# Kernel optimization log

Measured on AMD Instinct MI355X. Metric: run time of the kernel, lower is better.

## Reference

```python
import jax, jax.numpy as jnp
import numpy as np

B, N, E, H = 4, 512, 512, 8
HD = E // H // 2            # 32; per-head value dim is 2*HD = 64
C_IN = 64                   # u_proj Conv2d in_channels
LAMBDA_INIT = 0.8 - 0.6 * float(np.exp(-0.3 * (28.0 / 28.0) * (1 - 1)))  # layer_idx=1, depth=28 -> 0.2
LN_EPS = 1e-5


def setup_inputs() -> dict:
    key = jax.random.key(0)
    ks = jax.random.split(key, 13)
    x = jax.random.normal(ks[0], (B, N, E), dtype=jnp.float32)
    u = jax.random.normal(ks[1], (B, N, N, C_IN), dtype=jnp.float32)
    umask = jax.random.randint(ks[2], (B, N, N, 2 * H), 0, 2).astype(bool)
    s = 0.02
    v_w = jax.random.normal(ks[3], (E, E), dtype=jnp.float32) * s        # nn.Linear weight [out,in]
    out_w = jax.random.normal(ks[4], (E, E), dtype=jnp.float32) * s
    uproj_w = jax.random.normal(ks[5], (2 * H, C_IN), dtype=jnp.float32) * s  # 1x1 conv kernel
    uproj_b = jax.random.normal(ks[6], (2 * H,), dtype=jnp.float32) * s
    lq1 = jax.random.normal(ks[7], (E,), dtype=jnp.float32) * 0.1
    lk1 = jax.random.normal(ks[8], (E,), dtype=jnp.float32) * 0.1
    lq2 = jax.random.normal(ks[9], (E,), dtype=jnp.float32) * 0.1
    lk2 = jax.random.normal(ks[10], (E,), dtype=jnp.float32) * 0.1
    ln_w = jnp.ones((2 * HD,), dtype=jnp.float32)
    ln_b = jnp.zeros((2 * HD,), dtype=jnp.float32)
    return {"x": x, "u": u, "umask": umask, "v_w": v_w, "out_w": out_w,
            "uproj_w": uproj_w, "uproj_b": uproj_b,
            "lq1": lq1, "lk1": lk1, "lq2": lq2, "lk2": lk2,
            "ln_w": ln_w, "ln_b": ln_b}


def reference(x, u, umask, v_w, out_w, uproj_w, uproj_b, lq1, lk1, lq2, lk2, ln_w, ln_b):
    b, n, e = x.shape
    # v projection -> [B, H, N, 2*HD]
    v = jnp.einsum('bne,fe->bnf', x, v_w).reshape(b, n, H, 2 * HD).transpose(0, 2, 1, 3)
    # 1x1 conv on u: [B,N,N,C_IN] -> [B,N,N,2H]
    ue = jnp.einsum('bnmc,hc->bnmh', u, uproj_w) + uproj_b
    ue = jnp.where(umask, -jnp.inf, ue)
    # transpose(3,1): [B,N,N,2H] -> [B,2H,N,N]; softmax over last (key) axis
    aw = jax.nn.softmax(jnp.transpose(ue, (0, 3, 2, 1)), axis=-1)
    lam1 = jnp.exp(jnp.sum(lq1 * lk1))
    lam2 = jnp.exp(jnp.sum(lq2 * lk2))
    lam = lam1 - lam2 + LAMBDA_INIT
    aw = aw.reshape(b, H, 2, n, n)
    diff = aw[:, :, 0] - lam * aw[:, :, 1]          # [B,H,N,N]
    attn = jnp.einsum('bhnm,bhmd->bhnd', diff, v)   # [B,H,N,2HD]
    # sub-LayerNorm over last dim
    mu = jnp.mean(attn, axis=-1, keepdims=True)
    var = jnp.mean(jnp.square(attn - mu), axis=-1, keepdims=True)
    attn = (attn - mu) * jax.lax.rsqrt(var + LN_EPS) * ln_w + ln_b
    attn = attn.transpose(0, 2, 1, 3).reshape(b, n, e)
    return jnp.einsum('bne,fe->bnf', attn, out_w)
```

## Files before the change

kernel.cpp:

```cpp
#include <hip/hip_runtime.h>
#include <math.h>

typedef _Float16 f16x8 __attribute__((ext_vector_type(8)));
typedef _Float16 f16x4 __attribute__((ext_vector_type(4)));
typedef float    f32x4 __attribute__((ext_vector_type(4)));

constexpr int kB  = 4;
constexpr int kN  = 512;
constexpr int kE  = 512;
constexpr int kH  = 8;
constexpr int kH2 = 16;
constexpr int kC  = 64;
constexpr int kDV = 64;
constexpr float kLamInit = 0.2f;

__global__ __launch_bounds__(256) void prep_kernel(
    const float* __restrict__ x, const float* __restrict__ vw,
    const float* __restrict__ ow,
    const float* __restrict__ lq1, const float* __restrict__ lk1,
    const float* __restrict__ lq2, const float* __restrict__ lk2,
    _Float16* __restrict__ x16, _Float16* __restrict__ w16v,
    _Float16* __restrict__ w16o, float* __restrict__ lam_out) {
  const int bid = blockIdx.x;
  if (bid < 1536) {
    const float* src; _Float16* dst; int base;
    if (bid < 1024)      { src = x;  dst = x16;  base = bid; }
    else if (bid < 1280) { src = vw; dst = w16v; base = bid - 1024; }
    else                 { src = ow; dst = w16o; base = bid - 1280; }
    const int i = base * 256 + threadIdx.x;
    const float4 v = ((const float4*)src)[i];
    union { _Float16 h[4]; uint2 u2; } P;
    P.h[0]=(_Float16)v.x; P.h[1]=(_Float16)v.y;
    P.h[2]=(_Float16)v.z; P.h[3]=(_Float16)v.w;
    *(uint2*)(dst + i * 4) = P.u2;
  } else if (threadIdx.x < 64) {
    float s1 = 0.f, s2 = 0.f;
    for (int i = threadIdx.x; i < kE; i += 64) { s1 += lq1[i]*lk1[i]; s2 += lq2[i]*lk2[i]; }
    #pragma unroll
    for (int o = 32; o; o >>= 1) { s1 += __shfl_xor(s1, o); s2 += __shfl_xor(s2, o); }
    if (threadIdx.x == 0) lam_out[0] = expf(s1) - expf(s2) + kLamInit;
  }
}

__global__ __launch_bounds__(256) void hgemm16f(const _Float16* __restrict__ A16,
                                                const _Float16* __restrict__ W16,
                                                float* __restrict__ C,
                                                int M, int F, int K) {
  const int tid = threadIdx.x, lane = tid & 63, wv = tid >> 6;
  const int l15 = lane & 15, l4 = lane >> 4;
  const int m0 = blockIdx.y * 64 + wv * 16;
  const int f0 = blockIdx.x * 64;
  f32x4 acc[4] = {{0,0,0,0},{0,0,0,0},{0,0,0,0},{0,0,0,0}};
  const _Float16* Ap = A16 + (size_t)(m0 + l15) * K + l4 * 8;
  const _Float16* Wp = W16 + (size_t)(f0 + l15) * K + l4 * 8;
  for (int k0 = 0; k0 < K; k0 += 32) {
    const f16x8 af = *(const f16x8*)(Ap + k0);
    #pragma unroll
    for (int t = 0; t < 4; ++t) {
      const f16x8 bf = *(const f16x8*)(Wp + (size_t)t * 16 * K + k0);
      acc[t] = __builtin_amdgcn_mfma_f32_16x16x32_f16(af, bf, acc[t], 0, 0, 0);
    }
  }
  #pragma unroll
  for (int t = 0; t < 4; ++t)
    #pragma unroll
    for (int r = 0; r < 4; ++r)
      C[(size_t)(m0 + l4 * 4 + r) * F + f0 + t * 16 + l15] = acc[t][r];
}

__global__ __launch_bounds__(256) void hgemmT_v(const _Float16* __restrict__ W16,
                                                const _Float16* __restrict__ X16,
                                                _Float16* __restrict__ Vt) {
  const int tid = threadIdx.x, lane = tid & 63, wv = tid >> 6;
  const int l15 = lane & 15, l4 = lane >> 4;
  const int f0 = blockIdx.y * 64 + wv * 16;
  const int n0 = blockIdx.x * 64;
  f32x4 acc[4] = {{0,0,0,0},{0,0,0,0},{0,0,0,0},{0,0,0,0}};
  const _Float16* Ap = W16 + (size_t)(f0 + l15) * kE + l4 * 8;
  const _Float16* Bp = X16 + (size_t)(n0 + l15) * kE + l4 * 8;
  for (int k0 = 0; k0 < kE; k0 += 32) {
    const f16x8 af = *(const f16x8*)(Ap + k0);
    #pragma unroll
    for (int t = 0; t < 4; ++t) {
      const f16x8 bf = *(const f16x8*)(Bp + (size_t)t * 16 * kE + k0);
      acc[t] = __builtin_amdgcn_mfma_f32_16x16x32_f16(af, bf, acc[t], 0, 0, 0);
    }
  }
  #pragma unroll
  for (int t = 0; t < 4; ++t)
    #pragma unroll
    for (int r = 0; r < 4; ++r) {
      const int f  = f0 + l4 * 4 + r;
      const int ng = n0 + t * 16 + l15;
      const int bb = ng >> 9, n = ng & 511;
      Vt[(((size_t)((bb * kH + (f >> 6)) * kDV) + (f & 63)) * kN) + n] = (_Float16)acc[t][r];
    }
}

__global__ __launch_bounds__(512, 4) void fused_attn4(
    const float* __restrict__ u, const int* __restrict__ umask,
    const float* __restrict__ uw, const float* __restrict__ ub,
    const _Float16* __restrict__ Vt,
    _Float16* __restrict__ Opart, float* __restrict__ Spart) {
  __shared__ _Float16 P[16 * 648];
  __shared__ float S_lds[8][16][17];
  const int tid = threadIdx.x, lane = tid & 63, wv = tid >> 6;
  const int l15 = lane & 15, l4 = lane >> 4;
  const int qt = blockIdx.x, kh = blockIdx.y, b = blockIdx.z;
  const int q0 = qt * 16;
  const int kstart = kh * 128;

  f16x8 bfrag[2];
  #pragma unroll
  for (int ch = 0; ch < 2; ++ch) {
    const float* wp = uw + l15 * 64 + ch * 32 + l4 * 8;
    const float4 wa = *(const float4*)wp;
    const float4 wb = *(const float4*)(wp + 4);
    f16x8 bf;
    bf[0]=(_Float16)wa.x; bf[1]=(_Float16)wa.y; bf[2]=(_Float16)wa.z; bf[3]=(_Float16)wa.w;
    bf[4]=(_Float16)wb.x; bf[5]=(_Float16)wb.y; bf[6]=(_Float16)wb.z; bf[7]=(_Float16)wb.w;
    bfrag[ch] = bf;
  }
  const float bias = ub[l15];

  float s_acc[4] = {};
  f32x4 oacc[2][4];
  #pragma unroll
  for (int s = 0; s < 2; ++s)
    #pragma unroll
    for (int d = 0; d < 4; ++d) oacc[s][d] = (f32x4){0,0,0,0};

  for (int t = 0; t < 4; ++t) {
    const int k0 = kstart + t * 32;
    _Float16 vals[4][4];
    #pragma unroll
    for (int kk = 0; kk < 4; ++kk) {
      const int k = k0 + wv * 4 + kk;
      const float* up = u + (((size_t)(b * kN + k)) * kN + q0 + l15) * kC + l4 * 8;
      f32x4 acc = {0.f, 0.f, 0.f, 0.f};
      #pragma unroll
      for (int ch = 0; ch < 2; ++ch) {
        const float4 a0 = *(const float4*)(up + ch * 32);
        const float4 a1 = *(const float4*)(up + ch * 32 + 4);
        f16x8 af;
        af[0]=(_Float16)a0.x; af[1]=(_Float16)a0.y; af[2]=(_Float16)a0.z; af[3]=(_Float16)a0.w;
        af[4]=(_Float16)a1.x; af[5]=(_Float16)a1.y; af[6]=(_Float16)a1.z; af[7]=(_Float16)a1.w;
        acc = __builtin_amdgcn_mfma_f32_16x16x32_f16(af, bfrag[ch], acc, 0, 0, 0);
      }
      const int* mrow = umask + (((size_t)(b * kN + k)) * kN + q0) * kH2 + l15;
      #pragma unroll
      for (int r = 0; r < 4; ++r) {
        const float e = mrow[(l4 * 4 + r) * kH2] ? 0.f : __expf(acc[r] + bias);
        s_acc[r] += e;
        vals[r][kk] = (_Float16)e;
      }
    }
    #pragma unroll
    for (int r = 0; r < 4; ++r) {
      union { _Float16 h[4]; uint2 u2; } PK;
      #pragma unroll
      for (int kk = 0; kk < 4; ++kk) PK.h[kk] = vals[r][kk];
      *(uint2*)&P[l15 * 648 + (l4 * 4 + r) * 40 + wv * 4] = PK.u2;
    }
    __syncthreads();
    f16x8 va[4];
    #pragma unroll
    for (int dt = 0; dt < 4; ++dt)
      va[dt] = *(const f16x8*)(Vt + (((size_t)((b * kH + wv) * kDV + dt * 16 + l15)) * kN) + k0 + l4 * 8);
    #pragma unroll
    for (int s = 0; s < 2; ++s) {
      const f16x8 pb = *(const f16x8*)&P[(wv * 2 + s) * 648 + l15 * 40 + l4 * 8];
      #pragma unroll
      for (int dt = 0; dt < 4; ++dt)
        oacc[s][dt] = __builtin_amdgcn_mfma_f32_16x16x32_f16(va[dt], pb, oacc[s][dt], 0, 0, 0);
    }
    __syncthreads();
  }

  #pragma unroll
  for (int r = 0; r < 4; ++r) S_lds[wv][l15][l4 * 4 + r] = s_acc[r];
  __syncthreads();
  const int blk = (b * 4 + kh) * 32 + qt;
  if (tid < 256) {
    const int h2 = tid >> 4, q = tid & 15;
    float S = 0.f;
    #pragma unroll
    for (int j = 0; j < 8; ++j) S += S_lds[j][h2][q];
    Spart[(size_t)blk * 256 + h2 * 16 + q] = S;
  }
  _Float16* ob = Opart + (size_t)blk * 16384;
  #pragma unroll
  for (int s = 0; s < 2; ++s)
    #pragma unroll
    for (int dt = 0; dt < 4; ++dt)
      #pragma unroll
      for (int r = 0; r < 4; ++r)
        ob[((size_t)(s * 8 + wv) * 64 + dt * 16 + l4 * 4 + r) * 16 + l15] =
            (_Float16)oacc[s][dt][r];
}

__global__ __launch_bounds__(256) void combine3(
    const _Float16* __restrict__ Opart, const float* __restrict__ Spart,
    const float* __restrict__ lam_p, const float* __restrict__ ln_w,
    const float* __restrict__ ln_b, _Float16* __restrict__ a16) {
  __shared__ float vsh[64][17];
  __shared__ float inv_sh[2][16];
  const int tid = threadIdx.x;
  const int qt = blockIdx.x, h = blockIdx.y, b = blockIdx.z;
  if (tid < 32) {
    const int s = tid >> 4, q = tid & 15;
    float S = 0.f;
    #pragma unroll
    for (int kh = 0; kh < 4; ++kh)
      S += Spart[(size_t)((b * 4 + kh) * 32 + qt) * 256 + (h * 2 + s) * 16 + q];
    inv_sh[s][q] = (s ? lam_p[0] : 1.0f) / S;
  }
  float a0[4] = {}, a1[4] = {};
  #pragma unroll
  for (int kh = 0; kh < 4; ++kh) {
    const size_t base = (size_t)((b * 4 + kh) * 32 + qt) * 16384;
    const f16x4 p0 = *(const f16x4*)(Opart + base + (size_t)(0 * 8 + h) * 1024 + tid * 4);
    const f16x4 p1 = *(const f16x4*)(Opart + base + (size_t)(1 * 8 + h) * 1024 + tid * 4);
    #pragma unroll
    for (int j = 0; j < 4; ++j) { a0[j] += (float)p0[j]; a1[j] += (float)p1[j]; }
  }
  __syncthreads();
  {
    const int d = tid >> 2, q0i = (tid & 3) * 4;
    #pragma unroll
    for (int j = 0; j < 4; ++j)
      vsh[d][q0i + j] = a0[j] * inv_sh[0][q0i + j] - a1[j] * inv_sh[1][q0i + j];
  }
  __syncthreads();
  const int q = tid >> 4, i = tid & 15;
  float vv[4], s1 = 0.f, s2 = 0.f;
  #pragma unroll
  for (int jj = 0; jj < 4; ++jj) {
    vv[jj] = vsh[i * 4 + jj][q];
    s1 += vv[jj]; s2 += vv[jj] * vv[jj];
  }
  #pragma unroll
  for (int o = 1; o < 16; o <<= 1) { s1 += __shfl_xor(s1, o); s2 += __shfl_xor(s2, o); }
  const float mu = s1 * (1.0f / kDV);
  const float var = s2 * (1.0f / kDV) - mu * mu;
  const float rstd = rsqrtf(var + 1e-5f);
  union { _Float16 hh[4]; uint2 u2; } PK;
  #pragma unroll
  for (int jj = 0; jj < 4; ++jj)
    PK.hh[jj] = (_Float16)((vv[jj] - mu) * rstd * ln_w[i * 4 + jj] + ln_b[i * 4 + jj]);
  *(uint2*)(a16 + ((size_t)(b * kN + qt * 16 + q)) * kE + h * kDV + i * 4) = PK.u2;
}

extern "C" void kernel_launch(void* const* d_in, const int* in_sizes, int n_in,
                              void* d_out, int out_size, void* d_ws, size_t ws_size,
                              hipStream_t stream) {
  const float* x     = (const float*)d_in[0];
  const float* u     = (const float*)d_in[1];
  const int*   umask = (const int*)d_in[2];
  const float* v_w   = (const float*)d_in[3];
  const float* out_w = (const float*)d_in[4];
  const float* uw    = (const float*)d_in[5];
  const float* ubias = (const float*)d_in[6];
  const float* lq1   = (const float*)d_in[7];
  const float* lk1   = (const float*)d_in[8];
  const float* lq2   = (const float*)d_in[9];
  const float* lk2   = (const float*)d_in[10];
  const float* ln_w  = (const float*)d_in[11];
  const float* ln_b  = (const float*)d_in[12];
  float* out = (float*)d_out;

  char* ws = (char*)d_ws;
  const size_t sz_half = (size_t)kB * kN * kE * 2;
  const size_t sz_w16  = (size_t)kE * kE * 2;
  const size_t sz_op   = (size_t)512 * 16384 * 2;
  const size_t sz_sp   = (size_t)512 * 256 * 4;
  const size_t off_x16 = 256;
  const size_t off_wv  = off_x16 + sz_half;
  const size_t off_wo  = off_wv + sz_w16;
  const size_t off_vt  = off_wo + sz_w16;
  const size_t off_a16 = off_vt + sz_half;
  const size_t off_op  = off_a16 + sz_half;
  const size_t off_sp  = off_op + sz_op;
  if (ws_size < off_sp + sz_sp) return;
  float*    lam   = (float*)(ws);
  _Float16* x16   = (_Float16*)(ws + off_x16);
  _Float16* w16v  = (_Float16*)(ws + off_wv);
  _Float16* w16o  = (_Float16*)(ws + off_wo);
  _Float16* Vt    = (_Float16*)(ws + off_vt);
  _Float16* a16   = (_Float16*)(ws + off_a16);
  _Float16* Opart = (_Float16*)(ws + off_op);
  float*    Spart = (float*)(ws + off_sp);

  prep_kernel<<<dim3(1537), dim3(256), 0, stream>>>(
      x, v_w, out_w, lq1, lk1, lq2, lk2, x16, w16v, w16o, lam);
  hgemmT_v<<<dim3(32, 8), dim3(256), 0, stream>>>(w16v, x16, Vt);
  fused_attn4<<<dim3(kN / 16, 4, kB), dim3(512), 0, stream>>>(
      u, umask, uw, ubias, Vt, Opart, Spart);
  combine3<<<dim3(kN / 16, kH, kB), dim3(256), 0, stream>>>(
      Opart, Spart, lam, ln_w, ln_b, a16);
  hgemm16f<<<dim3(kE / 64, (kB * kN) / 64), dim3(256), 0, stream>>>(
      a16, w16o, out, kB * kN, kE, kE);
}
```

Baseline: 119.8 us.

## Pack umask into bitmasks in prep, widen attention k-steps, shrink GEMM tiles

The prep kernel now compacts the int32 umask into 16-bit per-(b,k,q) bitmasks, so the fused attention kernel reads 8 bytes per row group instead of scattered 4-byte ints. The attention kernel processes 64 keys per step instead of 32, halving the number of barrier pairs at the cost of a larger LDS tile. The two projection GEMMs switch to one 16x16 tile per wave, giving four times more blocks for better occupancy but less operand reuse. The full int mask is still read once in prep, and the packed mask adds an extra write and read.

```diff
diff --git a/kernel.cpp b/kernel.cpp
--- a/kernel.cpp
+++ b/kernel.cpp
@@ -14,13 +14,14 @@
 constexpr int kDV = 64;
 constexpr float kLamInit = 0.2f;
 
-__global__ __launch_bounds__(256) void prep_kernel(
+__global__ __launch_bounds__(256) void prep2_kernel(
     const float* __restrict__ x, const float* __restrict__ vw,
-    const float* __restrict__ ow,
+    const float* __restrict__ ow, const int* __restrict__ umask,
     const float* __restrict__ lq1, const float* __restrict__ lk1,
     const float* __restrict__ lq2, const float* __restrict__ lk2,
     _Float16* __restrict__ x16, _Float16* __restrict__ w16v,
-    _Float16* __restrict__ w16o, float* __restrict__ lam_out) {
+    _Float16* __restrict__ w16o, unsigned short* __restrict__ mbits,
+    float* __restrict__ lam_out) {
   const int bid = blockIdx.x;
   if (bid < 1536) {
     const float* src; _Float16* dst; int base;
@@ -33,76 +34,81 @@
     P.h[0]=(_Float16)v.x; P.h[1]=(_Float16)v.y;
     P.h[2]=(_Float16)v.z; P.h[3]=(_Float16)v.w;
     *(uint2*)(dst + i * 4) = P.u2;
-  } else if (threadIdx.x < 64) {
-    float s1 = 0.f, s2 = 0.f;
-    for (int i = threadIdx.x; i < kE; i += 64) { s1 += lq1[i]*lk1[i]; s2 += lq2[i]*lk2[i]; }
-    #pragma unroll
-    for (int o = 32; o; o >>= 1) { s1 += __shfl_xor(s1, o); s2 += __shfl_xor(s2, o); }
-    if (threadIdx.x == 0) lam_out[0] = expf(s1) - expf(s2) + kLamInit;
-  }
-}
-
-__global__ __launch_bounds__(256) void hgemm16f(const _Float16* __restrict__ A16,
-                                                const _Float16* __restrict__ W16,
-                                                float* __restrict__ C,
-                                                int M, int F, int K) {
+  } else if (bid == 1536) {
+    if (threadIdx.x < 64) {
+      float s1 = 0.f, s2 = 0.f;
+      for (int i = threadIdx.x; i < kE; i += 64) { s1 += lq1[i]*lk1[i]; s2 += lq2[i]*lk2[i]; }
+      #pragma unroll
+      for (int o = 32; o; o >>= 1) { s1 += __shfl_xor(s1, o); s2 += __shfl_xor(s2, o); }
+      if (threadIdx.x == 0) lam_out[0] = expf(s1) - expf(s2) + kLamInit;
+    }
+  } else {
+    const int i = (bid - 1537) * 256 + threadIdx.x;
+    const int4* src = (const int4*)(umask + (size_t)i * kH2);
+    unsigned int w = 0;
+    #pragma unroll
+    for (int c = 0; c < 4; ++c) {
+      const int4 m = src[c];
+      w |= (m.x & 1) << (c * 4 + 0);
+      w |= (m.y & 1) << (c * 4 + 1);
+      w |= (m.z & 1) << (c * 4 + 2);
+      w |= (m.w & 1) << (c * 4 + 3);
+    }
+    mbits[i] = (unsigned short)w;
+  }
+}
+
+__global__ __launch_bounds__(256, 4) void hgemm16f2(const _Float16* __restrict__ A16,
+                                                    const _Float16* __restrict__ W16,
+                                                    float* __restrict__ C,
+                                                    int M, int F, int K) {
   const int tid = threadIdx.x, lane = tid & 63, wv = tid >> 6;
   const int l15 = lane & 15, l4 = lane >> 4;
-  const int m0 = blockIdx.y * 64 + wv * 16;
-  const int f0 = blockIdx.x * 64;
-  f32x4 acc[4] = {{0,0,0,0},{0,0,0,0},{0,0,0,0},{0,0,0,0}};
+  const int m0 = blockIdx.y * 16;
+  const int f0 = blockIdx.x * 64 + wv * 16;
+  f32x4 acc = {0, 0, 0, 0};
   const _Float16* Ap = A16 + (size_t)(m0 + l15) * K + l4 * 8;
   const _Float16* Wp = W16 + (size_t)(f0 + l15) * K + l4 * 8;
   for (int k0 = 0; k0 < K; k0 += 32) {
     const f16x8 af = *(const f16x8*)(Ap + k0);
-    #pragma unroll
-    for (int t = 0; t < 4; ++t) {
-      const f16x8 bf = *(const f16x8*)(Wp + (size_t)t * 16 * K + k0);
-      acc[t] = __builtin_amdgcn_mfma_f32_16x16x32_f16(af, bf, acc[t], 0, 0, 0);
-    }
-  }
-  #pragma unroll
-  for (int t = 0; t < 4; ++t)
-    #pragma unroll
-    for (int r = 0; r < 4; ++r)
-      C[(size_t)(m0 + l4 * 4 + r) * F + f0 + t * 16 + l15] = acc[t][r];
-}
-
-__global__ __launch_bounds__(256) void hgemmT_v(const _Float16* __restrict__ W16,
-                                                const _Float16* __restrict__ X16,
-                                                _Float16* __restrict__ Vt) {
+    const f16x8 bf = *(const f16x8*)(Wp + k0);
+    acc = __builtin_amdgcn_mfma_f32_16x16x32_f16(af, bf, acc, 0, 0, 0);
+  }
+  #pragma unroll
+  for (int r = 0; r < 4; ++r)
+    C[(size_t)(m0 + l4 * 4 + r) * F + f0 + l15] = acc[r];
+}
+
+__global__ __launch_bounds__(256, 4) void hgemmT_v2(const _Float16* __restrict__ W16,
+                                                    const _Float16* __restrict__ X16,
+                                                    _Float16* __restrict__ Vt) {
   const int tid = threadIdx.x, lane = tid & 63, wv = tid >> 6;
   const int l15 = lane & 15, l4 = lane >> 4;
-  const int f0 = blockIdx.y * 64 + wv * 16;
-  const int n0 = blockIdx.x * 64;
-  f32x4 acc[4] = {{0,0,0,0},{0,0,0,0},{0,0,0,0},{0,0,0,0}};
+  const int f0 = blockIdx.y * 16;
+  const int n0 = blockIdx.x * 64 + wv * 16;
+  f32x4 acc = {0, 0, 0, 0};
   const _Float16* Ap = W16 + (size_t)(f0 + l15) * kE + l4 * 8;
   const _Float16* Bp = X16 + (size_t)(n0 + l15) * kE + l4 * 8;
   for (int k0 = 0; k0 < kE; k0 += 32) {
     const f16x8 af = *(const f16x8*)(Ap + k0);
-    #pragma unroll
-    for (int t = 0; t < 4; ++t) {
-      const f16x8 bf = *(const f16x8*)(Bp + (size_t)t * 16 * kE + k0);
-      acc[t] = __builtin_amdgcn_mfma_f32_16x16x32_f16(af, bf, acc[t], 0, 0, 0);
-    }
-  }
-  #pragma unroll
-  for (int t = 0; t < 4; ++t)
-    #pragma unroll
-    for (int r = 0; r < 4; ++r) {
-      const int f  = f0 + l4 * 4 + r;
-      const int ng = n0 + t * 16 + l15;
-      const int bb = ng >> 9, n = ng & 511;
-      Vt[(((size_t)((bb * kH + (f >> 6)) * kDV) + (f & 63)) * kN) + n] = (_Float16)acc[t][r];
-    }
-}
-
-__global__ __launch_bounds__(512, 4) void fused_attn4(
-    const float* __restrict__ u, const int* __restrict__ umask,
+    const f16x8 bf = *(const f16x8*)(Bp + k0);
+    acc = __builtin_amdgcn_mfma_f32_16x16x32_f16(af, bf, acc, 0, 0, 0);
+  }
+  #pragma unroll
+  for (int r = 0; r < 4; ++r) {
+    const int f  = f0 + l4 * 4 + r;
+    const int ng = n0 + l15;
+    const int bb = ng >> 9, n = ng & 511;
+    Vt[(((size_t)((bb * kH + (f >> 6)) * kDV) + (f & 63)) * kN) + n] = (_Float16)acc[r];
+  }
+}
+
+__global__ __launch_bounds__(512, 4) void fused_attn5(
+    const float* __restrict__ u, const unsigned short* __restrict__ mbits,
     const float* __restrict__ uw, const float* __restrict__ ub,
     const _Float16* __restrict__ Vt,
     _Float16* __restrict__ Opart, float* __restrict__ Spart) {
-  __shared__ _Float16 P[16 * 648];
+  __shared__ _Float16 P[16 * 1160];
   __shared__ float S_lds[8][16][17];
   const int tid = threadIdx.x, lane = tid & 63, wv = tid >> 6;
   const int l15 = lane & 15, l4 = lane >> 4;
@@ -130,12 +136,12 @@
     #pragma unroll
     for (int d = 0; d < 4; ++d) oacc[s][d] = (f32x4){0,0,0,0};
 
-  for (int t = 0; t < 4; ++t) {
-    const int k0 = kstart + t * 32;
-    _Float16 vals[4][4];
-    #pragma unroll
-    for (int kk = 0; kk < 4; ++kk) {
-      const int k = k0 + wv * 4 + kk;
+  for (int t = 0; t < 2; ++t) {
+    const int k0 = kstart + t * 64;
+    _Float16 vals[4][8];
+    #pragma unroll
+    for (int kk = 0; kk < 8; ++kk) {
+      const int k = k0 + wv * 8 + kk;
       const float* up = u + (((size_t)(b * kN + k)) * kN + q0 + l15) * kC + l4 * 8;
       f32x4 acc = {0.f, 0.f, 0.f, 0.f};
       #pragma unroll
@@ -147,32 +153,39 @@
         af[4]=(_Float16)a1.x; af[5]=(_Float16)a1.y; af[6]=(_Float16)a1.z; af[7]=(_Float16)a1.w;
         acc = __builtin_amdgcn_mfma_f32_16x16x32_f16(af, bfrag[ch], acc, 0, 0, 0);
       }
-      const int* mrow = umask + (((size_t)(b * kN + k)) * kN + q0) * kH2 + l15;
+      const unsigned long long w64 =
+          *(const unsigned long long*)(mbits + ((size_t)(b * kN + k)) * kN + q0 + l4 * 4);
       #pragma unroll
       for (int r = 0; r < 4; ++r) {
-        const float e = mrow[(l4 * 4 + r) * kH2] ? 0.f : __expf(acc[r] + bias);
+        const float e = ((w64 >> (r * 16 + l15)) & 1ULL) ? 0.f : __expf(acc[r] + bias);
         s_acc[r] += e;
         vals[r][kk] = (_Float16)e;
       }
     }
     #pragma unroll
     for (int r = 0; r < 4; ++r) {
-      union { _Float16 h[4]; uint2 u2; } PK;
-      #pragma unroll
-      for (int kk = 0; kk < 4; ++kk) PK.h[kk] = vals[r][kk];
-      *(uint2*)&P[l15 * 648 + (l4 * 4 + r) * 40 + wv * 4] = PK.u2;
+      union { _Float16 h[8]; int4 v; } PK;
+      #pragma unroll
+      for (int kk = 0; kk < 8; ++kk) PK.h[kk] = vals[r][kk];
+      *(int4*)&P[l15 * 1160 + (l4 * 4 + r) * 72 + wv * 8] = PK.v;
     }
     __syncthreads();
-    f16x8 va[4];
-    #pragma unroll
-    for (int dt = 0; dt < 4; ++dt)
-      va[dt] = *(const f16x8*)(Vt + (((size_t)((b * kH + wv) * kDV + dt * 16 + l15)) * kN) + k0 + l4 * 8);
+    f16x8 va[2][4];
+    #pragma unroll
+    for (int hf = 0; hf < 2; ++hf)
+      #pragma unroll
+      for (int dt = 0; dt < 4; ++dt)
+        va[hf][dt] = *(const f16x8*)(Vt + (((size_t)((b * kH + wv) * kDV + dt * 16 + l15)) * kN)
+                                     + k0 + hf * 32 + l4 * 8);
     #pragma unroll
     for (int s = 0; s < 2; ++s) {
-      const f16x8 pb = *(const f16x8*)&P[(wv * 2 + s) * 648 + l15 * 40 + l4 * 8];
-      #pragma unroll
-      for (int dt = 0; dt < 4; ++dt)
-        oacc[s][dt] = __builtin_amdgcn_mfma_f32_16x16x32_f16(va[dt], pb, oacc[s][dt], 0, 0, 0);
+      #pragma unroll
+      for (int hf = 0; hf < 2; ++hf) {
+        const f16x8 pb = *(const f16x8*)&P[(wv * 2 + s) * 1160 + l15 * 72 + hf * 32 + l4 * 8];
+        #pragma unroll
+        for (int dt = 0; dt < 4; ++dt)
+          oacc[s][dt] = __builtin_amdgcn_mfma_f32_16x16x32_f16(va[hf][dt], pb, oacc[s][dt], 0, 0, 0);
+      }
     }
     __syncthreads();
   }
@@ -274,6 +287,7 @@
   const size_t sz_w16  = (size_t)kE * kE * 2;
   const size_t sz_op   = (size_t)512 * 16384 * 2;
   const size_t sz_sp   = (size_t)512 * 256 * 4;
+  const size_t sz_mb   = (size_t)kB * kN * kN * 2;
   const size_t off_x16 = 256;
   const size_t off_wv  = off_x16 + sz_half;
   const size_t off_wo  = off_wv + sz_w16;
@@ -281,7 +295,8 @@
   const size_t off_a16 = off_vt + sz_half;
   const size_t off_op  = off_a16 + sz_half;
   const size_t off_sp  = off_op + sz_op;
-  if (ws_size < off_sp + sz_sp) return;
+  const size_t off_mb  = off_sp + sz_sp;
+  if (ws_size < off_mb + sz_mb) return;
   float*    lam   = (float*)(ws);
   _Float16* x16   = (_Float16*)(ws + off_x16);
   _Float16* w16v  = (_Float16*)(ws + off_wv);
@@ -290,14 +305,15 @@
   _Float16* a16   = (_Float16*)(ws + off_a16);
   _Float16* Opart = (_Float16*)(ws + off_op);
   float*    Spart = (float*)(ws + off_sp);
-
-  prep_kernel<<<dim3(1537), dim3(256), 0, stream>>>(
-      x, v_w, out_w, lq1, lk1, lq2, lk2, x16, w16v, w16o, lam);
-  hgemmT_v<<<dim3(32, 8), dim3(256), 0, stream>>>(w16v, x16, Vt);
-  fused_attn4<<<dim3(kN / 16, 4, kB), dim3(512), 0, stream>>>(
-      u, umask, uw, ubias, Vt, Opart, Spart);
+  unsigned short* mbits = (unsigned short*)(ws + off_mb);
+
+  prep2_kernel<<<dim3(5633), dim3(256), 0, stream>>>(
+      x, v_w, out_w, umask, lq1, lk1, lq2, lk2, x16, w16v, w16o, mbits, lam);
+  hgemmT_v2<<<dim3(32, 32), dim3(256), 0, stream>>>(w16v, x16, Vt);
+  fused_attn5<<<dim3(kN / 16, 4, kB), dim3(512), 0, stream>>>(
+      u, mbits, uw, ubias, Vt, Opart, Spart);
   combine3<<<dim3(kN / 16, kH, kB), dim3(256), 0, stream>>>(
       Opart, Spart, lam, ln_w, ln_b, a16);
-  hgemm16f<<<dim3(kE / 64, (kB * kN) / 64), dim3(256), 0, stream>>>(
+  hgemm16f2<<<dim3(kE / 64, (kB * kN) / 16), dim3(256), 0, stream>>>(
       a16, w16o, out, kB * kN, kE, kE);
 }
```

Result: no change. 122.1 us (+1.9%).
